# Performance work log

Measured on AMD Instinct MI355X. Metric: run time of the kernel, lower is better.

Reference implementation:

```python
import jax, jax.numpy as jnp
import numpy as np

MODEL_DIM = 128
NUM_HEADS = 8

def setup_inputs() -> dict:
    key = jax.random.key(0)
    kx, kq, kk, kv = jax.random.split(key, 4)
    B, S, D, H = 4, 2048, MODEL_DIM, NUM_HEADS
    scale = 1.0 / np.sqrt(D)
    x = jax.random.normal(kx, (B, S, D), dtype=jnp.float32)
    # nn.Linear weights: shape [out_features, in_features] = [H*D, D]
    W_q = jax.random.normal(kq, (H * D, D), dtype=jnp.float32) * scale
    W_k = jax.random.normal(kk, (H * D, D), dtype=jnp.float32) * scale
    W_v = jax.random.normal(kv, (H * D, D), dtype=jnp.float32) * scale
    return {"x": x, "W_q": W_q, "W_k": W_k, "W_v": W_v}

def reference(x, W_q, W_k, W_v):
    B, S, D = x.shape
    H = NUM_HEADS
    # projections: y = x @ W.T, then split heads -> [B, H, S, D]
    def proj(W):
        y = jnp.einsum('bsd,ed->bse', x, W)  # [B, S, H*D]
        return y.reshape(B, S, H, D).transpose(0, 2, 1, 3)
    Q, K, V = proj(W_q), proj(W_k), proj(W_v)
    # scores [B, H, S, S]
    A = jnp.einsum('bhsd,bhtd->bhst', Q, K) / jnp.sqrt(jnp.asarray(D, x.dtype))
    # AV then softmax over the model_dim axis (as in original: softmax after matmul)
    Z = jax.nn.softmax(jnp.einsum('bhst,bhtd->bhsd', A, V), axis=-1)
    return Z
```

## Files before the change

kernel.cpp:

```cpp
#include <hip/hip_runtime.h>
#include <hip/hip_bf16.h>


#define NB 4
#define NS 2048
#define ND 128
#define NH 8
#define EPB (NS * ND)

typedef unsigned short u16;
typedef unsigned int u32;
typedef short bf16x8 __attribute__((ext_vector_type(8)));
typedef float f32x4 __attribute__((ext_vector_type(4)));

struct __align__(8) us4 { u16 a, b, c, d; };

__device__ __forceinline__ void splitf(float f, u16& hi, u16& lo) {
    u32 fb = __float_as_uint(f);
    u32 hb = fb + 0x7FFFu + ((fb >> 16) & 1u);
    hi = (u16)(hb >> 16);
    float fh = __uint_as_float((hb >> 16) << 16);
    float fl = f - fh;
    u32 lb = __float_as_uint(fl);
    u32 lr = lb + 0x7FFFu + ((lb >> 16) & 1u);
    lo = (u16)(lr >> 16);
}

__global__ __launch_bounds__(256) void proj_kernel(
    const float* __restrict__ xg, const float* __restrict__ Wqg,
    const float* __restrict__ Wkg, const float* __restrict__ Wvg,
    u16* __restrict__ ws, int b0, int nbh)
{
    __shared__ float xsT[64][68];
    __shared__ float wsT[64][68];

    const int which = blockIdx.z;
    const float* __restrict__ W = (which == 0) ? Wqg : (which == 1) ? Wkg : Wvg;

    const int tid = threadIdx.x;
    const int bgl = blockIdx.x >> 5;
    const int sL0 = (blockIdx.x & 31) * 64;
    const int eL0 = blockIdx.y * 64;
    const int mG0 = (b0 + bgl) * NS + sL0;
    const int tr = tid >> 4;
    const int tc = tid & 15;

    float acc[4][4];
    #pragma unroll
    for (int i = 0; i < 4; ++i)
        #pragma unroll
        for (int j = 0; j < 4; ++j) acc[i][j] = 0.f;

    for (int kk = 0; kk < 2; ++kk) {
        __syncthreads();
        #pragma unroll
        for (int i = 0; i < 4; ++i) {
            int f  = tid + i * 256;
            int r  = f & 63;
            int kg = f >> 6;
            float4 xv = *(const float4*)&xg[(size_t)(mG0 + r) * ND + kk * 64 + kg * 4];
            xsT[kg * 4 + 0][r] = xv.x;
            xsT[kg * 4 + 1][r] = xv.y;
            xsT[kg * 4 + 2][r] = xv.z;
            xsT[kg * 4 + 3][r] = xv.w;
            float4 wv = *(const float4*)&W[(size_t)(eL0 + r) * ND + kk * 64 + kg * 4];
            wsT[kg * 4 + 0][r] = wv.x;
            wsT[kg * 4 + 1][r] = wv.y;
            wsT[kg * 4 + 2][r] = wv.z;
            wsT[kg * 4 + 3][r] = wv.w;
        }
        __syncthreads();
        #pragma unroll 4
        for (int k = 0; k < 64; ++k) {
            const float4 a = *(const float4*)&xsT[k][tr * 4];
            const float4 b = *(const float4*)&wsT[k][tc * 4];
            acc[0][0] += a.x * b.x; acc[0][1] += a.x * b.y; acc[0][2] += a.x * b.z; acc[0][3] += a.x * b.w;
            acc[1][0] += a.y * b.x; acc[1][1] += a.y * b.y; acc[1][2] += a.y * b.z; acc[1][3] += a.y * b.w;
            acc[2][0] += a.z * b.x; acc[2][1] += a.z * b.y; acc[2][2] += a.z * b.z; acc[2][3] += a.z * b.w;
            acc[3][0] += a.w * b.x; acc[3][1] += a.w * b.y; acc[3][2] += a.w * b.z; acc[3][3] += a.w * b.w;
        }
    }

    u16 hv[4][4], lv[4][4];
    #pragma unroll
    for (int i = 0; i < 4; ++i)
        #pragma unroll
        for (int j = 0; j < 4; ++j) splitf(acc[i][j], hv[i][j], lv[i][j]);

    const int e0t = eL0 + 4 * tc;
    const int hh  = e0t >> 7;
    const int d0  = e0t & 127;
    const int bhl = bgl * NH + hh;
    u16* hiB = ws + (size_t)(2 * which + 0) * nbh * EPB + (size_t)bhl * EPB;
    u16* loB = ws + (size_t)(2 * which + 1) * nbh * EPB + (size_t)bhl * EPB;

    if (which != 2) {
        const int kc = d0 >> 5, g = (d0 >> 3) & 3, j0 = d0 & 7;
        #pragma unroll
        for (int i = 0; i < 4; ++i) {
            const int s = sL0 + 4 * tr + i;
            size_t flat;
            if (which == 0) {
                const int q16 = s >> 4, c = s & 15;
                flat = ((size_t)(q16 * 4 + kc) * 64 + g * 16 + c) * 8 + j0;
            } else {
                const int T = s >> 5, nt = (s >> 4) & 1, c = s & 15;
                flat = ((size_t)((T * 4 + kc) * 2 + nt) * 64 + g * 16 + c) * 8 + j0;
            }
            us4 h4 = { hv[i][0], hv[i][1], hv[i][2], hv[i][3] };
            us4 l4 = { lv[i][0], lv[i][1], lv[i][2], lv[i][3] };
            *(us4*)(hiB + flat) = h4;
            *(us4*)(loB + flat) = l4;
        }
    } else {
        const int s0 = sL0 + 4 * tr;
        const int T = s0 >> 5, gp = (s0 >> 3) & 3, jt0 = s0 & 7;
        #pragma unroll
        for (int j = 0; j < 4; ++j) {
            const int d = d0 + j;
            const int ni = d >> 4, cV = d & 15;
            size_t flat = ((size_t)(T * 8 + ni) * 64 + gp * 16 + cV) * 8 + jt0;
            us4 h4 = { hv[0][j], hv[1][j], hv[2][j], hv[3][j] };
            us4 l4 = { lv[0][j], lv[1][j], lv[2][j], lv[3][j] };
            *(us4*)(hiB + flat) = h4;
            *(us4*)(loB + flat) = l4;
        }
    }
}

#define MFMA(a, b, c) __builtin_amdgcn_mfma_f32_16x16x32_bf16((a), (b), (c), 0, 0, 0)

__global__ __launch_bounds__(256, 2) void attn_kernel(
    const u16* __restrict__ ws, float* __restrict__ outg, int b0, int nbh)
{
    __shared__ __align__(16) u16 sKH[4096];
    __shared__ __align__(16) u16 sKL[4096];
    __shared__ __align__(16) u16 sVH[4096];
    __shared__ __align__(16) u16 sVL[4096];
    __shared__ u32 sP[4][33 * 32];

    const int tid = threadIdx.x;
    const int Wv = tid >> 6;
    const int l  = tid & 63;
    const int c  = l & 15;
    const int g  = l >> 4;
    const int bhl = blockIdx.y;
    const size_t tb = (size_t)bhl * EPB;
    const size_t TS = (size_t)nbh * EPB;

    const u16* QH = ws;
    const u16* QL = ws + TS;
    const u16* KH = ws + 2 * TS;
    const u16* KL = ws + 3 * TS;
    const u16* VH = ws + 4 * TS;
    const u16* VL = ws + 5 * TS;

    const int qb = blockIdx.x * 128 + Wv * 32;

    bf16x8 qh[2][4], ql[2][4];
    #pragma unroll
    for (int mi = 0; mi < 2; ++mi)
        #pragma unroll
        for (int kc = 0; kc < 4; ++kc) {
            size_t f = tb + ((size_t)(((qb + 16 * mi) >> 4) * 4 + kc) * 64 + l) * 8;
            qh[mi][kc] = *(const bf16x8*)(QH + f);
            ql[mi][kc] = *(const bf16x8*)(QL + f);
        }

    f32x4 z[2][8];
    #pragma unroll
    for (int mi = 0; mi < 2; ++mi)
        #pragma unroll
        for (int ni = 0; ni < 8; ++ni) z[mi][ni] = (f32x4){0.f, 0.f, 0.f, 0.f};

    u32* sPW = &sP[Wv][0];
    const float scale = 0.08838834764831845f;

    for (int T = 0; T < 64; ++T) {
        const size_t off = tb + (size_t)T * 4096;
        const uint4* gKH = (const uint4*)(KH + off);
        const uint4* gKL = (const uint4*)(KL + off);
        const uint4* gVH = (const uint4*)(VH + off);
        const uint4* gVL = (const uint4*)(VL + off);
        uint4 r0 = gKH[tid], r1 = gKH[tid + 256];
        uint4 r2 = gKL[tid], r3 = gKL[tid + 256];
        uint4 r4 = gVH[tid], r5 = gVH[tid + 256];
        uint4 r6 = gVL[tid], r7 = gVL[tid + 256];
        __syncthreads();
        ((uint4*)sKH)[tid] = r0; ((uint4*)sKH)[tid + 256] = r1;
        ((uint4*)sKL)[tid] = r2; ((uint4*)sKL)[tid + 256] = r3;
        ((uint4*)sVH)[tid] = r4; ((uint4*)sVH)[tid + 256] = r5;
        ((uint4*)sVL)[tid] = r6; ((uint4*)sVL)[tid + 256] = r7;
        __syncthreads();

        f32x4 s[2][2];
        #pragma unroll
        for (int mi = 0; mi < 2; ++mi)
            #pragma unroll
            for (int nt = 0; nt < 2; ++nt) s[mi][nt] = (f32x4){0.f, 0.f, 0.f, 0.f};
        #pragma unroll
        for (int kc = 0; kc < 4; ++kc) {
            bf16x8 kh0 = *(const bf16x8*)(sKH + ((kc * 2 + 0) * 64 + l) * 8);
            bf16x8 kh1 = *(const bf16x8*)(sKH + ((kc * 2 + 1) * 64 + l) * 8);
            bf16x8 kl0 = *(const bf16x8*)(sKL + ((kc * 2 + 0) * 64 + l) * 8);
            bf16x8 kl1 = *(const bf16x8*)(sKL + ((kc * 2 + 1) * 64 + l) * 8);
            #pragma unroll
            for (int mi = 0; mi < 2; ++mi) {
                s[mi][0] = MFMA(qh[mi][kc], kh0, s[mi][0]);
                s[mi][0] = MFMA(qh[mi][kc], kl0, s[mi][0]);
                s[mi][0] = MFMA(ql[mi][kc], kh0, s[mi][0]);
                s[mi][1] = MFMA(qh[mi][kc], kh1, s[mi][1]);
                s[mi][1] = MFMA(qh[mi][kc], kl1, s[mi][1]);
                s[mi][1] = MFMA(ql[mi][kc], kh1, s[mi][1]);
            }
        }

        #pragma unroll
        for (int mi = 0; mi < 2; ++mi)
            #pragma unroll
            for (int nt = 0; nt < 2; ++nt)
                #pragma unroll
                for (int r = 0; r < 4; ++r) {
                    float p = s[mi][nt][r] * scale;
                    u16 ph, pl; splitf(p, ph, pl);
                    sPW[(nt * 16 + c) * 33 + mi * 16 + g * 4 + r] = (u32)ph | ((u32)pl << 16);
                }

        bf16x8 pa_h[2], pa_l[2];
        #pragma unroll
        for (int mi = 0; mi < 2; ++mi)
            #pragma unroll
            for (int j = 0; j < 8; ++j) {
                u32 v = sPW[(8 * g + j) * 33 + mi * 16 + c];
                pa_h[mi][j] = (short)(v & 0xFFFFu);
                pa_l[mi][j] = (short)(v >> 16);
            }

        #pragma unroll
        for (int ni = 0; ni < 8; ++ni) {
            bf16x8 vh = *(const bf16x8*)(sVH + (ni * 64 + l) * 8);
            bf16x8 vl = *(const bf16x8*)(sVL + (ni * 64 + l) * 8);
            #pragma unroll
            for (int mi = 0; mi < 2; ++mi) {
                z[mi][ni] = MFMA(pa_h[mi], vh, z[mi][ni]);
                z[mi][ni] = MFMA(pa_h[mi], vl, z[mi][ni]);
                z[mi][ni] = MFMA(pa_l[mi], vh, z[mi][ni]);
            }
        }
    }

    const size_t obase = (size_t)(b0 * NH + bhl) * EPB;
    #pragma unroll
    for (int mi = 0; mi < 2; ++mi)
        #pragma unroll
        for (int r = 0; r < 4; ++r) {
            float v[8];
            float m = -3.4e38f;
            #pragma unroll
            for (int ni = 0; ni < 8; ++ni) { v[ni] = z[mi][ni][r]; m = fmaxf(m, v[ni]); }
            #pragma unroll
            for (int off = 1; off < 16; off <<= 1) m = fmaxf(m, __shfl_xor(m, off, 64));
            float sum = 0.f;
            #pragma unroll
            for (int ni = 0; ni < 8; ++ni) { v[ni] = expf(v[ni] - m); sum += v[ni]; }
            #pragma unroll
            for (int off = 1; off < 16; off <<= 1) sum += __shfl_xor(sum, off, 64);
            const float inv = 1.f / sum;
            const int q = qb + 16 * mi + 4 * g + r;
            #pragma unroll
            for (int ni = 0; ni < 8; ++ni)
                outg[obase + (size_t)q * ND + ni * 16 + c] = v[ni] * inv;
        }
}

extern "C" void kernel_launch(void* const* d_in, const int* in_sizes, int n_in,
                              void* d_out, int out_size, void* d_ws, size_t ws_size,
                              hipStream_t stream)
{
    (void)out_size;
    int xi = 0;
    for (int i = 0; i < n_in && i < 4; ++i)
        if (in_sizes[i] == NB * NS * ND) { xi = i; break; }
    const float* x = (const float*)d_in[xi];
    const float* Wsp[3]; int w = 0;
    for (int i = 0; i < 4; ++i) if (i != xi) Wsp[w++] = (const float*)d_in[i];
    const float* Wq = Wsp[0];
    const float* Wk = Wsp[1];
    const float* Wv = Wsp[2];
    float* out = (float*)d_out;
    u16* ws = (u16*)d_ws;

    auto slice_bytes = [](int nb) { return (size_t)6 * nb * NH * EPB * 2; };
    int nb = (ws_size >= slice_bytes(4)) ? 4 : (ws_size >= slice_bytes(2)) ? 2 : 1;
    const int nbh = nb * NH;

    for (int b0 = 0; b0 < NB; b0 += nb) {
        proj_kernel<<<dim3(nb * 32, 16, 3), dim3(256), 0, stream>>>(
            x, Wq, Wk, Wv, ws, b0, nbh);
        attn_kernel<<<dim3(16, nbh), dim3(256), 0, stream>>>(
            ws, out, b0, nbh);
    }
}
```

Before: 349.8 us.

## Double-buffer K/V tiles via async global-to-LDS loads in attention kernel

The attention kernel now stages K/V hi/lo tiles straight into LDS with global_load_lds into a double buffer, prefetching the next tile while the current one is computed, and synchronises with explicit vmcnt waits and barriers. It also shrinks the P scratch to a per-mi 32x17 layout, raises wave priority around MFMA blocks, and prefetches the projection kernel's second k-slice into registers during compute. This targets global-load latency stalls and register staging in the main loop, at the cost of doubled LDS (possibly lowering occupancy) and reliance on exact vmcnt counting.

After: 347.8 us. About the same (-0.6%).

```diff
diff --git a/kernel.cpp b/kernel.cpp
--- a/kernel.cpp
+++ b/kernel.cpp
@@ -14,6 +14,8 @@
 typedef float f32x4 __attribute__((ext_vector_type(4)));
 
 struct __align__(8) us4 { u16 a, b, c, d; };
+
+#define MFMA(a, b, c) __builtin_amdgcn_mfma_f32_16x16x32_bf16((a), (b), (c), 0, 0, 0)
 
 __device__ __forceinline__ void splitf(float f, u16& hi, u16& lo) {
     u32 fb = __float_as_uint(f);
@@ -26,6 +28,7 @@
     lo = (u16)(lr >> 16);
 }
 
+
 __global__ __launch_bounds__(256) void proj_kernel(
     const float* __restrict__ xg, const float* __restrict__ Wqg,
     const float* __restrict__ Wkg, const float* __restrict__ Wvg,
@@ -45,6 +48,16 @@
     const int tr = tid >> 4;
     const int tc = tid & 15;
 
+    const int fr = tid & 63;
+    const int fk = tid >> 6;
+
+    float4 xv[4], wv[4];
+    #pragma unroll
+    for (int i = 0; i < 4; ++i) {
+        xv[i] = *(const float4*)&xg[(size_t)(mG0 + fr) * ND + (fk + i * 4) * 4];
+        wv[i] = *(const float4*)&W[(size_t)(eL0 + fr) * ND + (fk + i * 4) * 4];
+    }
+
     float acc[4][4];
     #pragma unroll
     for (int i = 0; i < 4; ++i)
@@ -55,21 +68,24 @@
         __syncthreads();
         #pragma unroll
         for (int i = 0; i < 4; ++i) {
-            int f  = tid + i * 256;
-            int r  = f & 63;
-            int kg = f >> 6;
-            float4 xv = *(const float4*)&xg[(size_t)(mG0 + r) * ND + kk * 64 + kg * 4];
-            xsT[kg * 4 + 0][r] = xv.x;
-            xsT[kg * 4 + 1][r] = xv.y;
-            xsT[kg * 4 + 2][r] = xv.z;
-            xsT[kg * 4 + 3][r] = xv.w;
-            float4 wv = *(const float4*)&W[(size_t)(eL0 + r) * ND + kk * 64 + kg * 4];
-            wsT[kg * 4 + 0][r] = wv.x;
-            wsT[kg * 4 + 1][r] = wv.y;
-            wsT[kg * 4 + 2][r] = wv.z;
-            wsT[kg * 4 + 3][r] = wv.w;
+            int kg = fk + i * 4;
+            xsT[kg * 4 + 0][fr] = xv[i].x;
+            xsT[kg * 4 + 1][fr] = xv[i].y;
+            xsT[kg * 4 + 2][fr] = xv[i].z;
+            xsT[kg * 4 + 3][fr] = xv[i].w;
+            wsT[kg * 4 + 0][fr] = wv[i].x;
+            wsT[kg * 4 + 1][fr] = wv[i].y;
+            wsT[kg * 4 + 2][fr] = wv[i].z;
+            wsT[kg * 4 + 3][fr] = wv[i].w;
         }
         __syncthreads();
+        if (kk == 0) {
+            #pragma unroll
+            for (int i = 0; i < 4; ++i) {
+                xv[i] = *(const float4*)&xg[(size_t)(mG0 + fr) * ND + 64 + (fk + i * 4) * 4];
+                wv[i] = *(const float4*)&W[(size_t)(eL0 + fr) * ND + 64 + (fk + i * 4) * 4];
+            }
+        }
         #pragma unroll 4
         for (int k = 0; k < 64; ++k) {
             const float4 a = *(const float4*)&xsT[k][tr * 4];
@@ -91,28 +107,40 @@
     const int hh  = e0t >> 7;
     const int d0  = e0t & 127;
     const int bhl = bgl * NH + hh;
-    u16* hiB = ws + (size_t)(2 * which + 0) * nbh * EPB + (size_t)bhl * EPB;
-    u16* loB = ws + (size_t)(2 * which + 1) * nbh * EPB + (size_t)bhl * EPB;
-
-    if (which != 2) {
+    const size_t TS = (size_t)nbh * EPB;
+    const size_t tb = (size_t)bhl * EPB;
+
+    if (which == 0) {
+        u16* HB = ws + 0 * TS + tb;
+        u16* LB = ws + 1 * TS + tb;
         const int kc = d0 >> 5, g = (d0 >> 3) & 3, j0 = d0 & 7;
         #pragma unroll
         for (int i = 0; i < 4; ++i) {
             const int s = sL0 + 4 * tr + i;
-            size_t flat;
-            if (which == 0) {
-                const int q16 = s >> 4, c = s & 15;
-                flat = ((size_t)(q16 * 4 + kc) * 64 + g * 16 + c) * 8 + j0;
-            } else {
-                const int T = s >> 5, nt = (s >> 4) & 1, c = s & 15;
-                flat = ((size_t)((T * 4 + kc) * 2 + nt) * 64 + g * 16 + c) * 8 + j0;
-            }
+            const int q16 = s >> 4, c = s & 15;
+            size_t flat = ((size_t)(q16 * 4 + kc) * 64 + g * 16 + c) * 8 + j0;
             us4 h4 = { hv[i][0], hv[i][1], hv[i][2], hv[i][3] };
             us4 l4 = { lv[i][0], lv[i][1], lv[i][2], lv[i][3] };
-            *(us4*)(hiB + flat) = h4;
-            *(us4*)(loB + flat) = l4;
+            *(us4*)(HB + flat) = h4;
+            *(us4*)(LB + flat) = l4;
+        }
+    } else if (which == 1) {
+        u16* HB = ws + 2 * TS + tb;
+        u16* LB = ws + 3 * TS + tb;
+        const int kc = d0 >> 5, g = (d0 >> 3) & 3, j0 = d0 & 7;
+        #pragma unroll
+        for (int i = 0; i < 4; ++i) {
+            const int s = sL0 + 4 * tr + i;
+            const int T = s >> 5, nt = (s >> 4) & 1, c = s & 15;
+            size_t flat = ((size_t)((T * 4 + kc) * 2 + nt) * 64 + g * 16 + c) * 8 + j0;
+            us4 h4 = { hv[i][0], hv[i][1], hv[i][2], hv[i][3] };
+            us4 l4 = { lv[i][0], lv[i][1], lv[i][2], lv[i][3] };
+            *(us4*)(HB + flat) = h4;
+            *(us4*)(LB + flat) = l4;
         }
     } else {
+        u16* HB = ws + 4 * TS + tb;
+        u16* LB = ws + 5 * TS + tb;
         const int s0 = sL0 + 4 * tr;
         const int T = s0 >> 5, gp = (s0 >> 3) & 3, jt0 = s0 & 7;
         #pragma unroll
@@ -122,22 +150,17 @@
             size_t flat = ((size_t)(T * 8 + ni) * 64 + gp * 16 + cV) * 8 + jt0;
             us4 h4 = { hv[0][j], hv[1][j], hv[2][j], hv[3][j] };
             us4 l4 = { lv[0][j], lv[1][j], lv[2][j], lv[3][j] };
-            *(us4*)(hiB + flat) = h4;
-            *(us4*)(loB + flat) = l4;
+            *(us4*)(HB + flat) = h4;
+            *(us4*)(LB + flat) = l4;
         }
     }
 }
-
-#define MFMA(a, b, c) __builtin_amdgcn_mfma_f32_16x16x32_bf16((a), (b), (c), 0, 0, 0)
 
 __global__ __launch_bounds__(256, 2) void attn_kernel(
     const u16* __restrict__ ws, float* __restrict__ outg, int b0, int nbh)
 {
-    __shared__ __align__(16) u16 sKH[4096];
-    __shared__ __align__(16) u16 sKL[4096];
-    __shared__ __align__(16) u16 sVH[4096];
-    __shared__ __align__(16) u16 sVL[4096];
-    __shared__ u32 sP[4][33 * 32];
+    __shared__ __align__(16) u16 sbuf[2][4][4096];
+    __shared__ u32 sP[4][32 * 17];
 
     const int tid = threadIdx.x;
     const int Wv = tid >> 6;
@@ -149,7 +172,7 @@
     const size_t TS = (size_t)nbh * EPB;
 
     const u16* QH = ws;
-    const u16* QL = ws + TS;
+    const u16* QL = ws + 1 * TS;
     const u16* KH = ws + 2 * TS;
     const u16* KL = ws + 3 * TS;
     const u16* VH = ws + 4 * TS;
@@ -173,37 +196,53 @@
         #pragma unroll
         for (int ni = 0; ni < 8; ++ni) z[mi][ni] = (f32x4){0.f, 0.f, 0.f, 0.f};
 
+    const u16* srcs[4] = { KH, KL, VH, VL };
+    auto stage = [&](int buf, int T) {
+        #pragma unroll
+        for (int t4 = 0; t4 < 4; ++t4)
+            #pragma unroll
+            for (int r = 0; r < 2; ++r)
+                __builtin_amdgcn_global_load_lds(
+                    (const __attribute__((address_space(1))) void*)
+                        (srcs[t4] + tb + (size_t)T * 4096 + r * 2048 + tid * 8),
+                    (__attribute__((address_space(3))) void*)
+                        (&sbuf[buf][t4][r * 2048 + tid * 8]),
+                    16, 0, 0);
+    };
+
     u32* sPW = &sP[Wv][0];
     const float scale = 0.08838834764831845f;
 
+    stage(0, 0);
+
     for (int T = 0; T < 64; ++T) {
-        const size_t off = tb + (size_t)T * 4096;
-        const uint4* gKH = (const uint4*)(KH + off);
-        const uint4* gKL = (const uint4*)(KL + off);
-        const uint4* gVH = (const uint4*)(VH + off);
-        const uint4* gVL = (const uint4*)(VL + off);
-        uint4 r0 = gKH[tid], r1 = gKH[tid + 256];
-        uint4 r2 = gKL[tid], r3 = gKL[tid + 256];
-        uint4 r4 = gVH[tid], r5 = gVH[tid + 256];
-        uint4 r6 = gVL[tid], r7 = gVL[tid + 256];
-        __syncthreads();
-        ((uint4*)sKH)[tid] = r0; ((uint4*)sKH)[tid + 256] = r1;
-        ((uint4*)sKL)[tid] = r2; ((uint4*)sKL)[tid + 256] = r3;
-        ((uint4*)sVH)[tid] = r4; ((uint4*)sVH)[tid + 256] = r5;
-        ((uint4*)sVL)[tid] = r6; ((uint4*)sVL)[tid + 256] = r7;
-        __syncthreads();
+        const int cur = T & 1;
+        if (T < 63) {
+            stage(cur ^ 1, T + 1);
+            asm volatile("s_waitcnt vmcnt(8)" ::: "memory");
+        } else {
+            asm volatile("s_waitcnt vmcnt(0)" ::: "memory");
+        }
+        __builtin_amdgcn_s_barrier();
+        asm volatile("" ::: "memory");
+
+        const u16* bKH = &sbuf[cur][0][0];
+        const u16* bKL = &sbuf[cur][1][0];
+        const u16* bVH = &sbuf[cur][2][0];
+        const u16* bVL = &sbuf[cur][3][0];
 
         f32x4 s[2][2];
         #pragma unroll
         for (int mi = 0; mi < 2; ++mi)
             #pragma unroll
             for (int nt = 0; nt < 2; ++nt) s[mi][nt] = (f32x4){0.f, 0.f, 0.f, 0.f};
+        __builtin_amdgcn_s_setprio(1);
         #pragma unroll
         for (int kc = 0; kc < 4; ++kc) {
-            bf16x8 kh0 = *(const bf16x8*)(sKH + ((kc * 2 + 0) * 64 + l) * 8);
-            bf16x8 kh1 = *(const bf16x8*)(sKH + ((kc * 2 + 1) * 64 + l) * 8);
-            bf16x8 kl0 = *(const bf16x8*)(sKL + ((kc * 2 + 0) * 64 + l) * 8);
-            bf16x8 kl1 = *(const bf16x8*)(sKL + ((kc * 2 + 1) * 64 + l) * 8);
+            bf16x8 kh0 = *(const bf16x8*)(bKH + ((kc * 2 + 0) * 64 + l) * 8);
+            bf16x8 kh1 = *(const bf16x8*)(bKH + ((kc * 2 + 1) * 64 + l) * 8);
+            bf16x8 kl0 = *(const bf16x8*)(bKL + ((kc * 2 + 0) * 64 + l) * 8);
+            bf16x8 kl1 = *(const bf16x8*)(bKL + ((kc * 2 + 1) * 64 + l) * 8);
             #pragma unroll
             for (int mi = 0; mi < 2; ++mi) {
                 s[mi][0] = MFMA(qh[mi][kc], kh0, s[mi][0]);
@@ -214,32 +253,36 @@
                 s[mi][1] = MFMA(ql[mi][kc], kh1, s[mi][1]);
             }
         }
-
-        #pragma unroll
-        for (int mi = 0; mi < 2; ++mi)
+        __builtin_amdgcn_s_setprio(0);
+
+        bf16x8 pa_h[2], pa_l[2];
+        #pragma unroll
+        for (int mi = 0; mi < 2; ++mi) {
             #pragma unroll
             for (int nt = 0; nt < 2; ++nt)
                 #pragma unroll
                 for (int r = 0; r < 4; ++r) {
                     float p = s[mi][nt][r] * scale;
                     u16 ph, pl; splitf(p, ph, pl);
-                    sPW[(nt * 16 + c) * 33 + mi * 16 + g * 4 + r] = (u32)ph | ((u32)pl << 16);
+                    sPW[(nt * 16 + c) * 17 + 4 * g + r] = (u32)ph | ((u32)pl << 16);
                 }
-
-        bf16x8 pa_h[2], pa_l[2];
-        #pragma unroll
-        for (int mi = 0; mi < 2; ++mi)
+            union { u16 uh[8]; bf16x8 v; } ph8;
+            union { u16 ul[8]; bf16x8 v; } pl8;
             #pragma unroll
             for (int j = 0; j < 8; ++j) {
-                u32 v = sPW[(8 * g + j) * 33 + mi * 16 + c];
-                pa_h[mi][j] = (short)(v & 0xFFFFu);
-                pa_l[mi][j] = (short)(v >> 16);
+                u32 v = sPW[(8 * g + j) * 17 + c];
+                ph8.uh[j] = (u16)(v & 0xFFFFu);
+                pl8.ul[j] = (u16)(v >> 16);
             }
-
+            pa_h[mi] = ph8.v;
+            pa_l[mi] = pl8.v;
+        }
+
+        __builtin_amdgcn_s_setprio(1);
         #pragma unroll
         for (int ni = 0; ni < 8; ++ni) {
-            bf16x8 vh = *(const bf16x8*)(sVH + (ni * 64 + l) * 8);
-            bf16x8 vl = *(const bf16x8*)(sVL + (ni * 64 + l) * 8);
+            bf16x8 vh = *(const bf16x8*)(bVH + (ni * 64 + l) * 8);
+            bf16x8 vl = *(const bf16x8*)(bVL + (ni * 64 + l) * 8);
             #pragma unroll
             for (int mi = 0; mi < 2; ++mi) {
                 z[mi][ni] = MFMA(pa_h[mi], vh, z[mi][ni]);
@@ -247,6 +290,10 @@
                 z[mi][ni] = MFMA(pa_l[mi], vh, z[mi][ni]);
             }
         }
+        __builtin_amdgcn_s_setprio(0);
+
+        asm volatile("" ::: "memory");
+        __builtin_amdgcn_s_barrier();
     }
 
     const size_t obase = (size_t)(b0 * NH + bhl) * EPB;
```
